# Kernel optimization log

Measured on AMD Instinct MI355X. Metric: run time of the kernel, lower is better.

The kernel has to match this reference:

```python
import jax, jax.numpy as jnp
import numpy as np

B, L, D = 512, 64, 16          # batch, lookback, input channels
H, V = 256, 512                # hidden_dim, vector_field_dim
STEPS = 64                     # ode_steps (euler)
EPS = 1e-5


def setup_inputs() -> dict:
    key = jax.random.key(0)
    ks = jax.random.split(key, 8)
    s = lambda fan: 1.0 / np.sqrt(fan)
    return {
        "coeffs": jax.random.normal(ks[0], (B, L - 1, 4, D), jnp.float32) * 0.1,  # cubic spline (a,b,c,d) per interval
        "W0": jax.random.normal(ks[1], (H, D), jnp.float32) * s(D),
        "b0": jnp.zeros((H,), jnp.float32),
        "W1": jax.random.normal(ks[2], (V, H), jnp.float32) * s(H),
        "b1": jnp.zeros((V,), jnp.float32),
        "g1": jnp.ones((V,), jnp.float32),
        "be1": jnp.zeros((V,), jnp.float32),
        "W2": jax.random.normal(ks[3], (V, V), jnp.float32) * s(V),
        "b2": jnp.zeros((V,), jnp.float32),
        "g2": jnp.ones((V,), jnp.float32),
        "be2": jnp.zeros((V,), jnp.float32),
        "W3": jax.random.normal(ks[4], (H * D, V), jnp.float32) * s(V),
        "b3": jnp.zeros((H * D,), jnp.float32),
    }


def _layernorm(x, g, b):
    m = jnp.mean(x, axis=-1, keepdims=True)
    v = jnp.mean((x - m) ** 2, axis=-1, keepdims=True)
    return (x - m) * jax.lax.rsqrt(v + EPS) * g + b


def reference(coeffs, W0, b0, W1, b1, g1, be1, W2, b2, g2, be2, W3, b3):
    # initial projection: h0 = tanh(Linear(X(0))), X(0) = a-coeff of first interval
    X0 = coeffs[:, 0, 0, :]                      # (B, D)
    h0 = jnp.tanh(X0 @ W0.T + b0)                # (B, H)

    t_span = jnp.linspace(0.0, L - 1, STEPS + 1)
    dt = jnp.float32((L - 1) / STEPS)

    def vector_field(h):                         # f(h): (B,H) -> (B,H,D)
        z = jnp.tanh(h @ W1.T + b1)
        z = _layernorm(z, g1, be1)
        z = jnp.tanh(z @ W2.T + b2)
        z = _layernorm(z, g2, be2)
        out = z @ W3.T + b3                      # (B, H*D)
        return out.reshape(h.shape[0], H, D)

    def spline_deriv(t):                         # X'(t): (B, D)
        idx = jnp.clip(jnp.floor(t).astype(jnp.int32), 0, L - 2)
        c = jnp.take(coeffs, idx, axis=1)        # (B, 4, D)
        frac = t - idx.astype(t.dtype)
        return c[:, 1] + 2.0 * frac * c[:, 2] + 3.0 * (frac * frac) * c[:, 3]

    def step(h, t):                              # euler: h += f(h) @ dX
        dX = spline_deriv(t)                     # (B, D)
        h = h + jnp.einsum("bhd,bd->bh", vector_field(h), dX) * dt
        return h, None

    hT, _ = jax.lax.scan(step, h0, t_span[:-1])
    return hT                                    # (B, H) terminal hidden state
```

## Files before the change

### kernel.cpp

```cpp
#include <hip/hip_runtime.h>
#include <hip/hip_bf16.h>

#define B_   512
#define L_   64
#define D_   16
#define H_   256
#define V_   512
#define STEPS_ 64
#define DT_  0.984375f
#define LOSC 2048.0f
#define LOSC_INV (1.0f/2048.0f)

typedef _Float16 half_t;
typedef __attribute__((ext_vector_type(8))) _Float16 half8;
typedef __attribute__((ext_vector_type(4))) float f32x4;

__device__ __forceinline__ void split16(float x, half_t& hi, half_t& lo) {
    half_t h = (half_t)x;
    hi = h;
    lo = (half_t)((x - (float)h) * LOSC);
}


__global__ void pack_frag_kernel(const float* __restrict__ src, half_t* __restrict__ hi,
                                 half_t* __restrict__ lo, int Kc, int K, int total) {
    int idx = blockIdx.x * 256 + threadIdx.x;
    if (idx >= total) return;
    int j = idx & 7;
    int l = (idx >> 3) & 63;
    int gc = idx >> 9;
    int c = gc % Kc, g = gc / Kc;
    int n = (g << 4) + (l & 15);
    int k = (c << 5) + ((l >> 4) << 3) + j;
    float w = src[n * K + k];
    half_t h, lw;
    split16(w, h, lw);
    hi[idx] = h;
    lo[idx] = lw;
}

__global__ void pack_frag_scaled2_kernel(const float* __restrict__ src,
                                         const float* __restrict__ scale,
                                         half_t* __restrict__ hi, half_t* __restrict__ lo,
                                         int Kc, int K, int total) {
    int idx = blockIdx.x * 256 + threadIdx.x;
    if (idx >= total) return;
    int j = idx & 7;
    int l = (idx >> 3) & 63;
    int gc = idx >> 9;
    int c = gc % Kc, g = gc / Kc;
    int n = (g << 4) + (l & 15);
    int k = (c << 5) + ((l >> 4) << 3) + j;
    float w = src[n * K + k] * scale[k];
    half_t h, lw;
    split16(w, h, lw);
    hi[idx] = h;
    lo[idx] = lw;
}

__global__ void pack_frag_scaled1_kernel(const float* __restrict__ src,
                                         const float* __restrict__ scale,
                                         half_t* __restrict__ hi,
                                         int Kc, int K, int total) {
    int idx = blockIdx.x * 256 + threadIdx.x;
    if (idx >= total) return;
    int j = idx & 7;
    int l = (idx >> 3) & 63;
    int gc = idx >> 9;
    int c = gc % Kc, g = gc / Kc;
    int n = (g << 4) + (l & 15);
    int k = (c << 5) + ((l >> 4) << 3) + j;
    hi[idx] = (half_t)(src[n * K + k] * scale[k]);
}

__global__ void colvec_kernel(const float* __restrict__ W, const float* __restrict__ g,
                              const float* __restrict__ be, const float* __restrict__ b,
                              float* __restrict__ cg, float* __restrict__ cb, int N, int K) {
    int n = blockIdx.x * 4 + (threadIdx.x >> 6);
    if (n >= N) return;
    int l = threadIdx.x & 63;
    float sg = 0.f, sb = 0.f;
    for (int k = l; k < K; k += 64) {
        float w = W[n * K + k];
        sg += g[k] * w;
        sb += be[k] * w;
    }
    #pragma unroll
    for (int o = 32; o; o >>= 1) { sg += __shfl_xor(sg, o); sb += __shfl_xor(sb, o); }
    if (l == 0) { cg[n] = sg; cb[n] = sb + b[n]; }
}

__global__ void h0_kernel(const float* __restrict__ coeffs, const float* __restrict__ W0,
                          const float* __restrict__ b0, float* __restrict__ hout) {
    int b = blockIdx.x;
    int hh = threadIdx.x;
    float acc = b0[hh];
    #pragma unroll
    for (int d = 0; d < 16; d++)
        acc += coeffs[b * ((L_ - 1) * 4 * D_) + d] * W0[hh * 16 + d];
    hout[b * H_ + hh] = tanhf(acc);
}


__global__ __launch_bounds__(512) void gemm1_kernel(
    const float* __restrict__ hptr,
    const half_t* __restrict__ W1h, const half_t* __restrict__ W1l,
    const float* __restrict__ b1, half_t* __restrict__ t1,
    float* __restrict__ stats1, int sIdx)
{
    __shared__ __align__(16) half_t Ah[2 * 8 * 64 * 8];
    __shared__ __align__(16) half_t Al[2 * 8 * 64 * 8];
    __shared__ float zs[32][65];
    const int tid = threadIdx.x, w = tid >> 6, l = tid & 63;
    const int row0 = blockIdx.x * 32, col0 = blockIdx.y * 64;

    {
        int gm = w & 1;
        #pragma unroll
        for (int cc = 0; cc < 2; cc++) {
            int c = ((w >> 1) << 1) + cc;
            const float* src = hptr + (row0 + (gm << 4) + (l & 15)) * H_ + (c << 5) + ((l >> 4) << 3);
            float4 x = *(const float4*)src;
            float4 y = *(const float4*)(src + 4);
            float xx[8] = {x.x, x.y, x.z, x.w, y.x, y.y, y.z, y.w};
            half8 hv, lv;
            #pragma unroll
            for (int j = 0; j < 8; j++) { half_t a, b; split16(xx[j], a, b); hv[j] = a; lv[j] = b; }
            int base = (((gm << 3) + c) * 64 + l) * 8;
            *(half8*)&Ah[base] = hv;
            *(half8*)&Al[base] = lv;
        }
    }
    __syncthreads();

    const int mf = w & 1, nf = w >> 1;
    const int gn = (col0 >> 4) + nf;
    f32x4 acc = {0.f, 0.f, 0.f, 0.f}, accl = {0.f, 0.f, 0.f, 0.f};
    for (int c = 0; c < 8; c++) {
        half8 ah = *(const half8*)&Ah[(((mf << 3) + c) * 64 + l) * 8];
        half8 al = *(const half8*)&Al[(((mf << 3) + c) * 64 + l) * 8];
        half8 bh = *(const half8*)&W1h[(((gn << 3) + c) * 64 + l) * 8];
        half8 bl = *(const half8*)&W1l[(((gn << 3) + c) * 64 + l) * 8];
        acc  = __builtin_amdgcn_mfma_f32_16x16x32_f16(ah, bh, acc,  0, 0, 0);
        accl = __builtin_amdgcn_mfma_f32_16x16x32_f16(ah, bl, accl, 0, 0, 0);
        accl = __builtin_amdgcn_mfma_f32_16x16x32_f16(al, bh, accl, 0, 0, 0);
    }
    {
        int colb = (nf << 4) + (l & 15);
        float bb = b1[col0 + colb];
        #pragma unroll
        for (int j = 0; j < 4; j++) {
            float v = acc[j] + accl[j] * LOSC_INV + bb;
            zs[(mf << 4) + ((l >> 4) << 2) + j][colb] = tanhf(v);
        }
    }
    __syncthreads();
    {
        int r = tid >> 4, c0 = (tid & 15) << 2;
        float s = 0.f, ss = 0.f;
        #pragma unroll
        for (int j = 0; j < 4; j++) { float v = zs[r][c0 + j]; s += v; ss += v * v; }
        #pragma unroll
        for (int o = 8; o; o >>= 1) { s += __shfl_xor(s, o); ss += __shfl_xor(ss, o); }
        if ((tid & 15) == 0) {
            float* st = stats1 + (((sIdx << 3) + blockIdx.y) * 512 + row0 + r) * 2;
            st[0] = s; st[1] = ss;
        }
    }
    if (tid < 256) {
        int p = tid >> 6;
        int gmp = p & 1, cp = p >> 1;
        half8 hv;
        #pragma unroll
        for (int j = 0; j < 8; j++)
            hv[j] = (half_t)zs[(gmp << 4) + (l & 15)][(cp << 5) + ((l >> 4) << 3) + j];
        *(half8*)&t1[((((row0 >> 4) + gmp) * 16 + (col0 >> 5) + cp) * 64 + l) * 8] = hv;
    }
}

__global__ __launch_bounds__(512) void gemm2_kernel(
    const half_t* __restrict__ t1, const float* __restrict__ stats1,
    const half_t* __restrict__ W2gh, const half_t* __restrict__ W2gl,
    const float* __restrict__ cg2, const float* __restrict__ cb2,
    half_t* __restrict__ t2, float* __restrict__ stats2, int sIdx)
{
    __shared__ float zs[32][65];
    __shared__ float mr[32], rrs[32];
    const int tid = threadIdx.x, w = tid >> 6, l = tid & 63;
    const int row0 = blockIdx.x * 32, col0 = blockIdx.y * 64;

    if (tid < 32) {
        float s = 0.f, ss = 0.f;
        #pragma unroll
        for (int p = 0; p < 8; p++) {
            const float* st = stats1 + (((sIdx << 3) + p) * 512 + row0 + tid) * 2;
            s += st[0]; ss += st[1];
        }
        float m = s * (1.f / 512.f);
        mr[tid] = m;
        rrs[tid] = rsqrtf(ss * (1.f / 512.f) - m * m + 1e-5f);
    }
    __syncthreads();

    const int mf = w & 1, nf = w >> 1;
    const int gn = (col0 >> 4) + nf;
    const int gmA = (row0 >> 4) + mf;
    f32x4 acc = {0.f, 0.f, 0.f, 0.f}, accl = {0.f, 0.f, 0.f, 0.f};
    for (int c = 0; c < 16; c++) {
        half8 ah = *(const half8*)&t1[((gmA * 16 + c) * 64 + l) * 8];
        half8 bh = *(const half8*)&W2gh[(((gn << 4) + c) * 64 + l) * 8];
        half8 bl = *(const half8*)&W2gl[(((gn << 4) + c) * 64 + l) * 8];
        acc  = __builtin_amdgcn_mfma_f32_16x16x32_f16(ah, bh, acc,  0, 0, 0);
        accl = __builtin_amdgcn_mfma_f32_16x16x32_f16(ah, bl, accl, 0, 0, 0);
    }
    {
        int colb = (nf << 4) + (l & 15);
        int col = col0 + colb;
        float cgv = cg2[col], cbv = cb2[col];
        #pragma unroll
        for (int j = 0; j < 4; j++) {
            int r = (mf << 4) + ((l >> 4) << 2) + j;
            float S = acc[j] + accl[j] * LOSC_INV;
            float v = rrs[r] * S - mr[r] * rrs[r] * cgv + cbv;
            zs[r][colb] = tanhf(v);
        }
    }
    __syncthreads();
    {
        int r = tid >> 4, c0 = (tid & 15) << 2;
        float s = 0.f, ss = 0.f;
        #pragma unroll
        for (int j = 0; j < 4; j++) { float v = zs[r][c0 + j]; s += v; ss += v * v; }
        #pragma unroll
        for (int o = 8; o; o >>= 1) { s += __shfl_xor(s, o); ss += __shfl_xor(ss, o); }
        if ((tid & 15) == 0) {
            float* st = stats2 + (((sIdx << 3) + blockIdx.y) * 512 + row0 + r) * 2;
            st[0] = s; st[1] = ss;
        }
    }
    if (tid < 256) {
        int p = tid >> 6;
        int gmp = p & 1, cp = p >> 1;
        half8 hv;
        #pragma unroll
        for (int j = 0; j < 8; j++)
            hv[j] = (half_t)zs[(gmp << 4) + (l & 15)][(cp << 5) + ((l >> 4) << 3) + j];
        *(half8*)&t2[((((row0 >> 4) + gmp) * 16 + (col0 >> 5) + cp) * 64 + l) * 8] = hv;
    }
}

__global__ __launch_bounds__(512) void stage3_kernel(
    const half_t* __restrict__ t2, const float* __restrict__ stats2,
    const half_t* __restrict__ W3gh, const float* __restrict__ cg3,
    const float* __restrict__ cb3, const float* __restrict__ coeffs,
    float* __restrict__ hbuf, int ii, float frac, int sIdx)
{
    __shared__ float dxs[32][17];
    __shared__ float mvals[32], rvals[32];
    const int tid = threadIdx.x, w = tid >> 6, l = tid & 63;
    const int rg = blockIdx.x >> 5;
    const int cgi = blockIdx.x & 31;
    const int row0 = rg << 5;
    const int gn = (cgi << 3) + w;

    {
        int r = tid >> 4, d = tid & 15;
        int base = ((row0 + r) * (L_ - 1) + ii) * 64 + d;
        float c1 = coeffs[base + 16], c2 = coeffs[base + 32], c3 = coeffs[base + 48];
        dxs[r][d] = c1 + 2.0f * frac * c2 + 3.0f * (frac * frac) * c3;
    }
    if (tid < 32) {
        float s = 0.f, ss = 0.f;
        #pragma unroll
        for (int p = 0; p < 8; p++) {
            const float* st = stats2 + (((sIdx << 3) + p) * 512 + row0 + tid) * 2;
            s += st[0]; ss += st[1];
        }
        float m = s * (1.f / 512.f);
        mvals[tid] = m;
        rvals[tid] = rsqrtf(ss * (1.f / 512.f) - m * m + 1e-5f);
    }
    __syncthreads();

    const int gm0 = rg << 1;
    f32x4 acc0 = {0.f, 0.f, 0.f, 0.f}, acc1 = {0.f, 0.f, 0.f, 0.f};
    for (int c = 0; c < 16; c++) {
        half8 bh = *(const half8*)&W3gh[(((gn << 4) + c) * 64 + l) * 8];
        half8 a0 = *(const half8*)&t2[(((gm0 + 0) * 16 + c) * 64 + l) * 8];
        half8 a1 = *(const half8*)&t2[(((gm0 + 1) * 16 + c) * 64 + l) * 8];
        acc0 = __builtin_amdgcn_mfma_f32_16x16x32_f16(a0, bh, acc0, 0, 0, 0);
        acc1 = __builtin_amdgcn_mfma_f32_16x16x32_f16(a1, bh, acc1, 0, 0, 0);
    }

    const int d = l & 15;
    const int o = (gn << 4) + d;
    const float cgv = cg3[o], cbv = cb3[o];
    #pragma unroll
    for (int mf = 0; mf < 2; mf++) {
        f32x4 a = mf ? acc1 : acc0;
        #pragma unroll
        for (int j = 0; j < 4; j++) {
            int rl = (mf << 4) + ((l >> 4) << 2) + j;
            float vf = rvals[rl] * a[j] - mvals[rl] * rvals[rl] * cgv + cbv;
            float s = vf * dxs[rl][d];
            s += __shfl_xor(s, 1);
            s += __shfl_xor(s, 2);
            s += __shfl_xor(s, 4);
            s += __shfl_xor(s, 8);
            if (d == 0) hbuf[(row0 + rl) * H_ + gn] += s * DT_;
        }
    }
}


extern "C" void kernel_launch(void* const* d_in, const int* in_sizes, int n_in,
                              void* d_out, int out_size, void* d_ws, size_t ws_size,
                              hipStream_t stream) {
    const float* coeffs = (const float*)d_in[0];
    const float* W0  = (const float*)d_in[1];
    const float* b0  = (const float*)d_in[2];
    const float* W1  = (const float*)d_in[3];
    const float* b1  = (const float*)d_in[4];
    const float* g1  = (const float*)d_in[5];
    const float* be1 = (const float*)d_in[6];
    const float* W2  = (const float*)d_in[7];
    const float* b2  = (const float*)d_in[8];
    const float* g2  = (const float*)d_in[9];
    const float* be2 = (const float*)d_in[10];
    const float* W3  = (const float*)d_in[11];
    const float* b3  = (const float*)d_in[12];

    char* w = (char*)d_ws;
    float*  hbuf   = (float*)(w);
    half_t* t1     = (half_t*)(w + 524288);
    half_t* t2     = (half_t*)(w + 1048576);
    half_t* W1h    = (half_t*)(w + 1572864);
    half_t* W1l    = (half_t*)(w + 1835008);
    half_t* W2gh   = (half_t*)(w + 2097152);
    half_t* W2gl   = (half_t*)(w + 2621440);
    half_t* W3gh   = (half_t*)(w + 3145728);
    float*  cg2    = (float*)(w + 7340032);
    float*  cb2    = (float*)(w + 7342080);
    float*  cg3    = (float*)(w + 7344128);
    float*  cb3    = (float*)(w + 7360512);
    float*  stats1 = (float*)(w + 7376896);
    float*  stats2 = (float*)(w + 9474048);

    pack_frag_kernel<<<512, 256, 0, stream>>>(W1, W1h, W1l, 8, H_, V_ * H_);
    pack_frag_scaled2_kernel<<<1024, 256, 0, stream>>>(W2, g1, W2gh, W2gl, 16, V_, V_ * V_);
    pack_frag_scaled1_kernel<<<8192, 256, 0, stream>>>(W3, g2, W3gh, 16, V_, (H_ * D_) * V_);
    colvec_kernel<<<V_ / 4, 256, 0, stream>>>(W2, g1, be1, b2, cg2, cb2, V_, V_);
    colvec_kernel<<<(H_ * D_) / 4, 256, 0, stream>>>(W3, g2, be2, b3, cg3, cb3, H_ * D_, V_);
    h0_kernel<<<B_, H_, 0, stream>>>(coeffs, W0, b0, hbuf);

    for (int s = 0; s < STEPS_; s++) {
        float t = (float)s * 0.984375f;
        int ii = (int)t;
        if (ii > L_ - 2) ii = L_ - 2;
        float frac = t - (float)ii;
        gemm1_kernel<<<dim3(16, 8), 512, 0, stream>>>(hbuf, W1h, W1l, b1, t1, stats1, s);
        gemm2_kernel<<<dim3(16, 8), 512, 0, stream>>>(t1, stats1, W2gh, W2gl,
                                                      cg2, cb2, t2, stats2, s);
        stage3_kernel<<<512, 512, 0, stream>>>(t2, stats2, W3gh, cg3, cb3, coeffs,
                                               hbuf, ii, frac, s);
    }

    hipMemcpyAsync(d_out, hbuf, (size_t)B_ * H_ * sizeof(float),
                   hipMemcpyDeviceToDevice, stream);
}
```

Baseline: 1.514 ms.

## Fuse first two MLP GEMMs into one kernel with redundant full-row layer1

Merges the first-layer GEMM (with tanh and layernorm statistics) and the second-layer GEMM into a single kernel. Each block recomputes the full 512-wide first layer for its 32 rows so the layernorm can be finished locally, removing the t1/stats1 round trip and one kernel launch per Euler step. This makes the W1 work eight times redundant across column blocks and uses much more LDS per block. It also stages the t2 A-fragments in shared memory inside stage3 instead of reloading them from global memory.

```diff
diff --git a/kernel.cpp b/kernel.cpp
--- a/kernel.cpp
+++ b/kernel.cpp
@@ -101,18 +101,22 @@
     hout[b * H_ + hh] = tanhf(acc);
 }
 
-
-__global__ __launch_bounds__(512) void gemm1_kernel(
+__global__ __launch_bounds__(512) void mlpf_kernel(
     const float* __restrict__ hptr,
     const half_t* __restrict__ W1h, const half_t* __restrict__ W1l,
-    const float* __restrict__ b1, half_t* __restrict__ t1,
-    float* __restrict__ stats1, int sIdx)
+    const float* __restrict__ b1,
+    const half_t* __restrict__ W2gh, const half_t* __restrict__ W2gl,
+    const float* __restrict__ cg2, const float* __restrict__ cb2,
+    half_t* __restrict__ t2, float* __restrict__ stats2, int sIdx)
 {
-    __shared__ __align__(16) half_t Ah[2 * 8 * 64 * 8];
-    __shared__ __align__(16) half_t Al[2 * 8 * 64 * 8];
-    __shared__ float zs[32][65];
+    __shared__ __align__(16) half_t A1h[2 * 8 * 64 * 8];
+    __shared__ __align__(16) half_t A1l[2 * 8 * 64 * 8];
+    __shared__ float zs[32][522];
+    __shared__ __align__(16) half_t A2[2 * 16 * 64 * 8];
+    __shared__ float mr[32], rrs[32];
     const int tid = threadIdx.x, w = tid >> 6, l = tid & 63;
     const int row0 = blockIdx.x * 32, col0 = blockIdx.y * 64;
+    const int mf = w & 1;
 
     {
         int gm = w & 1;
@@ -127,92 +131,78 @@
             #pragma unroll
             for (int j = 0; j < 8; j++) { half_t a, b; split16(xx[j], a, b); hv[j] = a; lv[j] = b; }
             int base = (((gm << 3) + c) * 64 + l) * 8;
-            *(half8*)&Ah[base] = hv;
-            *(half8*)&Al[base] = lv;
-        }
-    }
-    __syncthreads();
-
-    const int mf = w & 1, nf = w >> 1;
-    const int gn = (col0 >> 4) + nf;
-    f32x4 acc = {0.f, 0.f, 0.f, 0.f}, accl = {0.f, 0.f, 0.f, 0.f};
+            *(half8*)&A1h[base] = hv;
+            *(half8*)&A1l[base] = lv;
+        }
+    }
+    __syncthreads();
+
+    f32x4 acc[8], accl[8];
+    #pragma unroll
+    for (int i = 0; i < 8; i++) { acc[i] = (f32x4){0,0,0,0}; accl[i] = (f32x4){0,0,0,0}; }
     for (int c = 0; c < 8; c++) {
-        half8 ah = *(const half8*)&Ah[(((mf << 3) + c) * 64 + l) * 8];
-        half8 al = *(const half8*)&Al[(((mf << 3) + c) * 64 + l) * 8];
-        half8 bh = *(const half8*)&W1h[(((gn << 3) + c) * 64 + l) * 8];
-        half8 bl = *(const half8*)&W1l[(((gn << 3) + c) * 64 + l) * 8];
-        acc  = __builtin_amdgcn_mfma_f32_16x16x32_f16(ah, bh, acc,  0, 0, 0);
-        accl = __builtin_amdgcn_mfma_f32_16x16x32_f16(ah, bl, accl, 0, 0, 0);
-        accl = __builtin_amdgcn_mfma_f32_16x16x32_f16(al, bh, accl, 0, 0, 0);
-    }
-    {
-        int colb = (nf << 4) + (l & 15);
-        float bb = b1[col0 + colb];
-        #pragma unroll
-        for (int j = 0; j < 4; j++) {
-            float v = acc[j] + accl[j] * LOSC_INV + bb;
-            zs[(mf << 4) + ((l >> 4) << 2) + j][colb] = tanhf(v);
-        }
-    }
-    __syncthreads();
-    {
-        int r = tid >> 4, c0 = (tid & 15) << 2;
+        half8 ah = *(const half8*)&A1h[(((mf << 3) + c) * 64 + l) * 8];
+        half8 al = *(const half8*)&A1l[(((mf << 3) + c) * 64 + l) * 8];
+        #pragma unroll
+        for (int i = 0; i < 8; i++) {
+            int gn = ((w >> 1) << 3) + i;
+            half8 bh = *(const half8*)&W1h[(((gn << 3) + c) * 64 + l) * 8];
+            half8 bl = *(const half8*)&W1l[(((gn << 3) + c) * 64 + l) * 8];
+            acc[i]  = __builtin_amdgcn_mfma_f32_16x16x32_f16(ah, bh, acc[i],  0, 0, 0);
+            accl[i] = __builtin_amdgcn_mfma_f32_16x16x32_f16(ah, bl, accl[i], 0, 0, 0);
+            accl[i] = __builtin_amdgcn_mfma_f32_16x16x32_f16(al, bh, accl[i], 0, 0, 0);
+        }
+    }
+    #pragma unroll
+    for (int i = 0; i < 8; i++) {
+        int gn = ((w >> 1) << 3) + i;
+        int col = (gn << 4) + (l & 15);
+        float bb = b1[col];
+        #pragma unroll
+        for (int j = 0; j < 4; j++)
+            zs[(mf << 4) + ((l >> 4) << 2) + j][col] = tanhf(acc[i][j] + accl[i][j] * LOSC_INV + bb);
+    }
+    __syncthreads();
+
+    {
+        int r = tid >> 4, q = tid & 15;
         float s = 0.f, ss = 0.f;
-        #pragma unroll
-        for (int j = 0; j < 4; j++) { float v = zs[r][c0 + j]; s += v; ss += v * v; }
+        for (int k = 0; k < 32; k++) {
+            float v = zs[r][q + (k << 4)];
+            s += v; ss += v * v;
+        }
         #pragma unroll
         for (int o = 8; o; o >>= 1) { s += __shfl_xor(s, o); ss += __shfl_xor(ss, o); }
-        if ((tid & 15) == 0) {
-            float* st = stats1 + (((sIdx << 3) + blockIdx.y) * 512 + row0 + r) * 2;
-            st[0] = s; st[1] = ss;
-        }
-    }
-    if (tid < 256) {
-        int p = tid >> 6;
-        int gmp = p & 1, cp = p >> 1;
+        if (q == 0) {
+            float m = s * (1.f / 512.f);
+            mr[r] = m;
+            rrs[r] = rsqrtf(ss * (1.f / 512.f) - m * m + 1e-5f);
+        }
+    }
+    #pragma unroll
+    for (int u = 0; u < 4; u++) {
+        int slot = (u << 9) + tid;
+        int gm = slot >> 10, rem = slot & 1023;
+        int c = rem >> 6, ll = rem & 63;
+        const float* srcz = &zs[(gm << 4) + (ll & 15)][(c << 5) + ((ll >> 4) << 3)];
         half8 hv;
         #pragma unroll
-        for (int j = 0; j < 8; j++)
-            hv[j] = (half_t)zs[(gmp << 4) + (l & 15)][(cp << 5) + ((l >> 4) << 3) + j];
-        *(half8*)&t1[((((row0 >> 4) + gmp) * 16 + (col0 >> 5) + cp) * 64 + l) * 8] = hv;
-    }
-}
-
-__global__ __launch_bounds__(512) void gemm2_kernel(
-    const half_t* __restrict__ t1, const float* __restrict__ stats1,
-    const half_t* __restrict__ W2gh, const half_t* __restrict__ W2gl,
-    const float* __restrict__ cg2, const float* __restrict__ cb2,
-    half_t* __restrict__ t2, float* __restrict__ stats2, int sIdx)
-{
-    __shared__ float zs[32][65];
-    __shared__ float mr[32], rrs[32];
-    const int tid = threadIdx.x, w = tid >> 6, l = tid & 63;
-    const int row0 = blockIdx.x * 32, col0 = blockIdx.y * 64;
-
-    if (tid < 32) {
-        float s = 0.f, ss = 0.f;
-        #pragma unroll
-        for (int p = 0; p < 8; p++) {
-            const float* st = stats1 + (((sIdx << 3) + p) * 512 + row0 + tid) * 2;
-            s += st[0]; ss += st[1];
-        }
-        float m = s * (1.f / 512.f);
-        mr[tid] = m;
-        rrs[tid] = rsqrtf(ss * (1.f / 512.f) - m * m + 1e-5f);
-    }
-    __syncthreads();
-
-    const int mf = w & 1, nf = w >> 1;
-    const int gn = (col0 >> 4) + nf;
-    const int gmA = (row0 >> 4) + mf;
-    f32x4 acc = {0.f, 0.f, 0.f, 0.f}, accl = {0.f, 0.f, 0.f, 0.f};
+        for (int j = 0; j < 8; j++) hv[j] = (half_t)srcz[j];
+        *(half8*)&A2[slot << 3] = hv;
+    }
+    __syncthreads();
+
+    const int nf = w >> 1;
+    const int gnO = (col0 >> 4) + nf;
+    f32x4 a2 = {0.f, 0.f, 0.f, 0.f}, a2l = {0.f, 0.f, 0.f, 0.f};
     for (int c = 0; c < 16; c++) {
-        half8 ah = *(const half8*)&t1[((gmA * 16 + c) * 64 + l) * 8];
-        half8 bh = *(const half8*)&W2gh[(((gn << 4) + c) * 64 + l) * 8];
-        half8 bl = *(const half8*)&W2gl[(((gn << 4) + c) * 64 + l) * 8];
-        acc  = __builtin_amdgcn_mfma_f32_16x16x32_f16(ah, bh, acc,  0, 0, 0);
-        accl = __builtin_amdgcn_mfma_f32_16x16x32_f16(ah, bl, accl, 0, 0, 0);
-    }
+        half8 ah = *(const half8*)&A2[(((mf << 4) + c) * 64 + l) * 8];
+        half8 bh = *(const half8*)&W2gh[(((gnO << 4) + c) * 64 + l) * 8];
+        half8 bl = *(const half8*)&W2gl[(((gnO << 4) + c) * 64 + l) * 8];
+        a2  = __builtin_amdgcn_mfma_f32_16x16x32_f16(ah, bh, a2,  0, 0, 0);
+        a2l = __builtin_amdgcn_mfma_f32_16x16x32_f16(ah, bl, a2l, 0, 0, 0);
+    }
+    __syncthreads();
     {
         int colb = (nf << 4) + (l & 15);
         int col = col0 + colb;
@@ -220,7 +210,7 @@
         #pragma unroll
         for (int j = 0; j < 4; j++) {
             int r = (mf << 4) + ((l >> 4) << 2) + j;
-            float S = acc[j] + accl[j] * LOSC_INV;
+            float S = a2[j] + a2l[j] * LOSC_INV;
             float v = rrs[r] * S - mr[r] * rrs[r] * cgv + cbv;
             zs[r][colb] = tanhf(v);
         }
@@ -255,6 +245,7 @@
     const float* __restrict__ cb3, const float* __restrict__ coeffs,
     float* __restrict__ hbuf, int ii, float frac, int sIdx)
 {
+    __shared__ __align__(16) half_t Ah[2 * 16 * 64 * 8];
     __shared__ float dxs[32][17];
     __shared__ float mvals[32], rvals[32];
     const int tid = threadIdx.x, w = tid >> 6, l = tid & 63;
@@ -262,6 +253,7 @@
     const int cgi = blockIdx.x & 31;
     const int row0 = rg << 5;
     const int gn = (cgi << 3) + w;
+    const int gm0 = rg << 1;
 
     {
         int r = tid >> 4, d = tid & 15;
@@ -280,14 +272,21 @@
         mvals[tid] = m;
         rvals[tid] = rsqrtf(ss * (1.f / 512.f) - m * m + 1e-5f);
     }
-    __syncthreads();
-
-    const int gm0 = rg << 1;
+    #pragma unroll
+    for (int u = 0; u < 4; u++) {
+        int slot = (u << 9) + tid;
+        int gmi = slot >> 10, rem = slot & 1023;
+        int c = rem >> 6, ll = rem & 63;
+        *(half8*)&Ah[slot << 3] =
+            *(const half8*)&t2[((((gm0 + gmi) << 4) + c) * 64 + ll) * 8];
+    }
+    __syncthreads();
+
     f32x4 acc0 = {0.f, 0.f, 0.f, 0.f}, acc1 = {0.f, 0.f, 0.f, 0.f};
     for (int c = 0; c < 16; c++) {
         half8 bh = *(const half8*)&W3gh[(((gn << 4) + c) * 64 + l) * 8];
-        half8 a0 = *(const half8*)&t2[(((gm0 + 0) * 16 + c) * 64 + l) * 8];
-        half8 a1 = *(const half8*)&t2[(((gm0 + 1) * 16 + c) * 64 + l) * 8];
+        half8 a0 = *(const half8*)&Ah[((c) * 64 + l) * 8];
+        half8 a1 = *(const half8*)&Ah[((16 + c) * 64 + l) * 8];
         acc0 = __builtin_amdgcn_mfma_f32_16x16x32_f16(a0, bh, acc0, 0, 0, 0);
         acc1 = __builtin_amdgcn_mfma_f32_16x16x32_f16(a1, bh, acc1, 0, 0, 0);
     }
@@ -332,19 +331,17 @@
 
     char* w = (char*)d_ws;
     float*  hbuf   = (float*)(w);
-    half_t* t1     = (half_t*)(w + 524288);
-    half_t* t2     = (half_t*)(w + 1048576);
-    half_t* W1h    = (half_t*)(w + 1572864);
-    half_t* W1l    = (half_t*)(w + 1835008);
-    half_t* W2gh   = (half_t*)(w + 2097152);
-    half_t* W2gl   = (half_t*)(w + 2621440);
-    half_t* W3gh   = (half_t*)(w + 3145728);
-    float*  cg2    = (float*)(w + 7340032);
-    float*  cb2    = (float*)(w + 7342080);
-    float*  cg3    = (float*)(w + 7344128);
-    float*  cb3    = (float*)(w + 7360512);
-    float*  stats1 = (float*)(w + 7376896);
-    float*  stats2 = (float*)(w + 9474048);
+    half_t* t2     = (half_t*)(w + 524288);
+    half_t* W1h    = (half_t*)(w + 1048576);
+    half_t* W1l    = (half_t*)(w + 1310720);
+    half_t* W2gh   = (half_t*)(w + 1572864);
+    half_t* W2gl   = (half_t*)(w + 2097152);
+    half_t* W3gh   = (half_t*)(w + 2621440);
+    float*  cg2    = (float*)(w + 6815744);
+    float*  cb2    = (float*)(w + 6817792);
+    float*  cg3    = (float*)(w + 6819840);
+    float*  cb3    = (float*)(w + 6836224);
+    float*  stats2 = (float*)(w + 6852608);
 
     pack_frag_kernel<<<512, 256, 0, stream>>>(W1, W1h, W1l, 8, H_, V_ * H_);
     pack_frag_scaled2_kernel<<<1024, 256, 0, stream>>>(W2, g1, W2gh, W2gl, 16, V_, V_ * V_);
@@ -358,9 +355,9 @@
         int ii = (int)t;
         if (ii > L_ - 2) ii = L_ - 2;
         float frac = t - (float)ii;
-        gemm1_kernel<<<dim3(16, 8), 512, 0, stream>>>(hbuf, W1h, W1l, b1, t1, stats1, s);
-        gemm2_kernel<<<dim3(16, 8), 512, 0, stream>>>(t1, stats1, W2gh, W2gl,
-                                                      cg2, cb2, t2, stats2, s);
+        mlpf_kernel<<<dim3(16, 8), 512, 0, stream>>>(hbuf, W1h, W1l, b1,
+                                                     W2gh, W2gl, cg2, cb2,
+                                                     t2, stats2, s);
         stage3_kernel<<<512, 512, 0, stream>>>(t2, stats2, W3gh, cg3, cb3, coeffs,
                                                hbuf, ii, frac, s);
     }
```

Measured after the change: 1.880 ms. +24.2%, slower.
